# Kernel optimization log

Measured on AMD Instinct MI355X. Metric: run time of the kernel, lower is better.

Reference implementation:

```python
import jax, jax.numpy as jnp
import numpy as np

N_ATOMS, N_UND, N_DIR, N_ANG, N_STRUCT = 8192, 65536, 131072, 262144, 128
FEA, NRAD, NANGB, NCONV = 64, 9, 9, 4

FLOAT_NAMES = ["bond_bases_ag", "bond_bases_bg", "angle_bases", "atom_emb", "Wb", "Wa",
               "Wbw_ag", "Wbw_bg",
               "ac_cw1", "ac_cb1", "ac_cw2", "ac_cb2", "ac_gw1", "ac_gb1", "ac_gw2", "ac_gb2", "ac_out",
               "bc_cw1", "bc_cb1", "bc_cw2", "bc_cb2", "bc_gw1", "bc_gb1", "bc_gw2", "bc_gb2", "bc_out",
               "an_cw", "an_cb", "an_gw", "an_gb",
               "ro_w1", "ro_b1", "ro_w2", "ro_b2", "ro_w3", "ro_b3"]
INT_NAMES = ["atomic_numbers", "atom_graph", "directed2undirected",
             "bond_graph_atoms", "bond_graph_bonds", "atom_owners"]


def _silu(x):
    return x * jax.nn.sigmoid(x)


def _gmlp(x, cw1, cb1, cw2, cb2, gw1, gb1, gw2, gb2):
    # GatedMLP (norm=None): silu(MLP_core(x)) * sigmoid(MLP_gate(x)), each MLP = Lin-silu-Lin
    core = _silu(_silu(x @ cw1 + cb1) @ cw2 + cb2)
    gate = jax.nn.sigmoid(_silu(x @ gw1 + gb1) @ gw2 + gb2)
    return core * gate


def _forward(F, I):
    seg = jax.ops.segment_sum
    atom = F["atom_emb"][I["atomic_numbers"]]            # [N, 64]
    bond = F["bond_bases_ag"] @ F["Wb"]                  # [U, 64]
    angle = F["angle_bases"] @ F["Wa"]                   # [A, 64]
    bw_ag = F["bond_bases_ag"] @ F["Wbw_ag"]             # [U, 64]
    bw_bg = F["bond_bases_bg"] @ F["Wbw_bg"]             # [U, 64]
    ag0, ag1 = I["atom_graph"][:, 0], I["atom_graph"][:, 1]
    d2u = I["directed2undirected"]
    bgi, bgj = I["bond_graph_bonds"][:, 0], I["bond_graph_bonds"][:, 1]
    bga = I["bond_graph_atoms"]

    def atom_conv(i, atom, bond):
        msg = jnp.concatenate([atom[ag0], bond[d2u], atom[ag1]], axis=1)   # [E, 192]
        msg = _gmlp(msg, F["ac_cw1"][i], F["ac_cb1"][i], F["ac_cw2"][i], F["ac_cb2"][i],
                    F["ac_gw1"][i], F["ac_gb1"][i], F["ac_gw2"][i], F["ac_gb2"][i])
        msg = msg * bw_ag[d2u]
        # scatter-add to center atoms, linear mlp_out (no bias), resnet
        return atom + seg(msg, ag0, num_segments=N_ATOMS) @ F["ac_out"][i]

    for i in range(NCONV - 1):
        atom = atom_conv(i, atom, bond)
        # BondConv over bond graph (angles)
        tot = jnp.concatenate([bond[bgi], bond[bgj], angle, atom[bga]], axis=1)  # [A, 256]
        upd = _gmlp(tot, F["bc_cw1"][i], F["bc_cb1"][i], F["bc_cw2"][i], F["bc_cb2"][i],
                    F["bc_gw1"][i], F["bc_gb1"][i], F["bc_gw2"][i], F["bc_gb2"][i])
        upd = upd * bw_bg[bgi]
        bond = bond + seg(upd, bgi, num_segments=N_UND) @ F["bc_out"][i]
        # AngleUpdate (hidden_dim=0 -> single linear in each gated branch), resnet
        tot2 = jnp.concatenate([bond[bgi], bond[bgj], angle, atom[bga]], axis=1)
        angle = angle + _silu(tot2 @ F["an_cw"][i] + F["an_cb"][i]) * \
            jax.nn.sigmoid(tot2 @ F["an_gw"][i] + F["an_gb"][i])
    atom = atom_conv(NCONV - 1, atom, bond)

    # mlp_first readout: per-atom energy MLP then average pooling per structure
    e = _silu(atom @ F["ro_w1"] + F["ro_b1"])
    e = _silu(e @ F["ro_w2"] + F["ro_b2"])
    e = (e @ F["ro_w3"] + F["ro_b3"])[:, 0]              # [N]
    owners = I["atom_owners"]
    esum = seg(e, owners, num_segments=N_STRUCT)
    cnt = seg(jnp.ones_like(e), owners, num_segments=N_STRUCT)
    return esum / jnp.maximum(cnt, 1.0)                  # [N_STRUCT] energy/atom


def setup_inputs() -> dict:
    key = jax.random.key(0)
    ks = iter(jax.random.split(key, 64))

    def nrm(shape, fan_in):
        return jax.random.normal(next(ks), shape, dtype=jnp.float32) / np.float32(np.sqrt(fan_in))

    z = lambda *s: jnp.zeros(s, dtype=jnp.float32)
    inp = {}
    inp["atomic_numbers"] = jax.random.randint(next(ks), (N_ATOMS,), 0, 94, dtype=jnp.int32)
    inp["bond_bases_ag"] = jax.random.uniform(next(ks), (N_UND, NRAD), dtype=jnp.float32)
    inp["bond_bases_bg"] = jax.random.uniform(next(ks), (N_UND, NRAD), dtype=jnp.float32)
    inp["angle_bases"] = jax.random.uniform(next(ks), (N_ANG, NANGB), dtype=jnp.float32)
    inp["atom_graph"] = jax.random.randint(next(ks), (N_DIR, 2), 0, N_ATOMS, dtype=jnp.int32)
    inp["directed2undirected"] = jax.random.randint(next(ks), (N_DIR,), 0, N_UND, dtype=jnp.int32)
    inp["bond_graph_atoms"] = jax.random.randint(next(ks), (N_ANG,), 0, N_ATOMS, dtype=jnp.int32)
    inp["bond_graph_bonds"] = jax.random.randint(next(ks), (N_ANG, 2), 0, N_UND, dtype=jnp.int32)
    inp["atom_owners"] = jnp.sort(jax.random.randint(next(ks), (N_ATOMS,), 0, N_STRUCT, dtype=jnp.int32))
    inp["atom_emb"] = nrm((95, FEA), 1.0)
    inp["Wb"] = nrm((NRAD, FEA), NRAD)
    inp["Wa"] = nrm((NANGB, FEA), NANGB)
    inp["Wbw_ag"] = nrm((NRAD, FEA), NRAD)
    inp["Wbw_bg"] = nrm((NRAD, FEA), NRAD)
    d_a, d_b = 3 * FEA, 4 * FEA
    nb = NCONV - 1
    inp["ac_cw1"] = nrm((NCONV, d_a, FEA), d_a); inp["ac_cb1"] = z(NCONV, FEA)
    inp["ac_cw2"] = nrm((NCONV, FEA, FEA), FEA); inp["ac_cb2"] = z(NCONV, FEA)
    inp["ac_gw1"] = nrm((NCONV, d_a, FEA), d_a); inp["ac_gb1"] = z(NCONV, FEA)
    inp["ac_gw2"] = nrm((NCONV, FEA, FEA), FEA); inp["ac_gb2"] = z(NCONV, FEA)
    inp["ac_out"] = nrm((NCONV, FEA, FEA), FEA)
    inp["bc_cw1"] = nrm((nb, d_b, FEA), d_b); inp["bc_cb1"] = z(nb, FEA)
    inp["bc_cw2"] = nrm((nb, FEA, FEA), FEA); inp["bc_cb2"] = z(nb, FEA)
    inp["bc_gw1"] = nrm((nb, d_b, FEA), d_b); inp["bc_gb1"] = z(nb, FEA)
    inp["bc_gw2"] = nrm((nb, FEA, FEA), FEA); inp["bc_gb2"] = z(nb, FEA)
    inp["bc_out"] = nrm((nb, FEA, FEA), FEA)
    inp["an_cw"] = nrm((nb, d_b, FEA), d_b); inp["an_cb"] = z(nb, FEA)
    inp["an_gw"] = nrm((nb, d_b, FEA), d_b); inp["an_gb"] = z(nb, FEA)
    inp["ro_w1"] = nrm((FEA, FEA), FEA); inp["ro_b1"] = z(FEA)
    inp["ro_w2"] = nrm((FEA, FEA), FEA); inp["ro_b2"] = z(FEA)
    inp["ro_w3"] = nrm((FEA, 1), FEA); inp["ro_b3"] = z(1)
    return inp


def reference(atomic_numbers, bond_bases_ag, bond_bases_bg, angle_bases, atom_graph,
              directed2undirected, bond_graph_atoms, bond_graph_bonds, atom_owners,
              atom_emb, Wb, Wa, Wbw_ag, Wbw_bg,
              ac_cw1, ac_cb1, ac_cw2, ac_cb2, ac_gw1, ac_gb1, ac_gw2, ac_gb2, ac_out,
              bc_cw1, bc_cb1, bc_cw2, bc_cb2, bc_gw1, bc_gb1, bc_gw2, bc_gb2, bc_out,
              an_cw, an_cb, an_gw, an_gb,
              ro_w1, ro_b1, ro_w2, ro_b2, ro_w3, ro_b3):
    loc = locals()
    F = {k: loc[k] for k in FLOAT_NAMES}
    I = {k: loc[k] for k in INT_NAMES}
    return _forward(F, I)
```

## Files before the change

kernel.cpp:

```cpp
#include <hip/hip_runtime.h>
#include <hip/hip_bf16.h>

typedef float f32x4 __attribute__((ext_vector_type(4)));
typedef short s16x8 __attribute__((ext_vector_type(8)));
typedef unsigned int u32x4 __attribute__((ext_vector_type(4)));

#define DEV static __device__ __forceinline__

DEV unsigned short f2bf(float x){
    unsigned u = __builtin_bit_cast(unsigned, x);
    u += 0x7FFFu + ((u >> 16) & 1u);
    return (unsigned short)(u >> 16);
}
DEV float bf2f(unsigned short h){
    unsigned u = ((unsigned)h) << 16;
    return __builtin_bit_cast(float, u);
}
DEV float sigm_(float x){ return __builtin_amdgcn_rcpf(1.0f + __expf(-x)); }
DEV float silu_(float x){ return x * sigm_(x); }

__global__ __launch_bounds__(256) void k_transconv(const float* __restrict__ src,
                                                   unsigned short* __restrict__ dst,
                                                   int K, int total){
    int gid = blockIdx.x * 256 + threadIdx.x;
    if (gid >= total) return;
    int kn  = K * 64;
    int b   = gid / kn;
    int rem = gid - b * kn;
    int k   = rem >> 6, n = rem & 63;
    dst[b * kn + n * K + k] = f2bf(src[gid]);
}

__global__ __launch_bounds__(256) void k_embed(const float* __restrict__ emb,
                                               const int* __restrict__ z,
                                               unsigned short* __restrict__ out){
    int gid = blockIdx.x * 256 + threadIdx.x;
    int n = gid >> 6, f = gid & 63;
    out[gid] = f2bf(emb[z[n] * 64 + f]);
}

__global__ __launch_bounds__(256) void k_smallmm(const float* __restrict__ bases,
                                                 const float* __restrict__ W,
                                                 unsigned short* __restrict__ out){
    int gid = blockIdx.x * 256 + threadIdx.x;
    int r = gid >> 6, f = gid & 63;
    const float* b = bases + r * 9;
    float acc = 0.f;
    #pragma unroll
    for (int k = 0; k < 9; ++k) acc += b[k] * W[k * 64 + f];
    out[gid] = f2bf(acc);
}

__global__ void k_count(const int* __restrict__ dst, int stride, int n, int* __restrict__ cnt){
    int i = blockIdx.x * 256 + threadIdx.x;
    if (i < n) atomicAdd(&cnt[dst[(size_t)i * stride]], 1);
}

__global__ __launch_bounds__(256) void k_bsum(const int* __restrict__ cnt,
                                              int* __restrict__ bsum){
    int i = blockIdx.x * 256 + threadIdx.x;
    int v = cnt[i];
    #pragma unroll
    for (int off = 32; off > 0; off >>= 1) v += __shfl_down(v, off);
    __shared__ int ws[4];
    if ((threadIdx.x & 63) == 0) ws[threadIdx.x >> 6] = v;
    __syncthreads();
    if (threadIdx.x == 0) bsum[blockIdx.x] = ws[0] + ws[1] + ws[2] + ws[3];
}

__global__ __launch_bounds__(256) void k_bscan(const int* __restrict__ bsum,
                                               int* __restrict__ bbase, int nb,
                                               int* __restrict__ total_out){
    __shared__ int sh[256];
    int t = threadIdx.x;
    int v = (t < nb) ? bsum[t] : 0;
    sh[t] = v;
    __syncthreads();
    for (int d = 1; d < 256; d <<= 1){
        int u = (t >= d) ? sh[t - d] : 0;
        __syncthreads();
        sh[t] += u;
        __syncthreads();
    }
    if (t < nb) bbase[t] = sh[t] - v;
    if (t == nb - 1) *total_out = sh[t];
}

__global__ __launch_bounds__(256) void k_offs(const int* __restrict__ cnt,
                                              const int* __restrict__ bbase,
                                              int* __restrict__ offs){
    __shared__ int sh[256];
    int t = threadIdx.x;
    int i = blockIdx.x * 256 + t;
    int v = cnt[i];
    sh[t] = v;
    __syncthreads();
    for (int d = 1; d < 256; d <<= 1){
        int u = (t >= d) ? sh[t - d] : 0;
        __syncthreads();
        sh[t] += u;
        __syncthreads();
    }
    offs[i] = bbase[blockIdx.x] + sh[t] - v;
}

__global__ void k_fill(const int* __restrict__ dst, int stride, int n,
                       const int* __restrict__ offs, int* __restrict__ cur,
                       int* __restrict__ idx){
    int i = blockIdx.x * 256 + threadIdx.x;
    if (i < n){
        int d = dst[(size_t)i * stride];
        int p = offs[d] + atomicAdd(&cur[d], 1);
        idx[p] = i;
    }
}

__global__ __launch_bounds__(256) void k_reduce(const unsigned short* __restrict__ upd,
                                                const int* __restrict__ offs,
                                                const int* __restrict__ idx,
                                                unsigned short* __restrict__ act, int nRows){
    int gid = blockIdx.x * 256 + threadIdx.x;
    int row = gid >> 3;
    if (row >= nRows) return;
    int c8 = (gid & 7) * 8;
    int o = offs[row], e = offs[row + 1];
    float acc[8] = {};
    for (int j = o; j < e; ++j){
        s16x8 v = *(const s16x8*)&upd[(size_t)idx[j] * 64 + c8];
        #pragma unroll
        for (int q = 0; q < 8; ++q) acc[q] += bf2f((unsigned short)v[q]);
    }
    s16x8 a = *(s16x8*)&act[(size_t)row * 64 + c8];
    #pragma unroll
    for (int q = 0; q < 8; ++q) a[q] = (short)f2bf(bf2f((unsigned short)a[q]) + acc[q]);
    *(s16x8*)&act[(size_t)row * 64 + c8] = a;
}

#define MFMA16(a,b,c) __builtin_amdgcn_mfma_f32_16x16x32_bf16(a,b,c,0,0,0)

__global__ __launch_bounds__(256, 4) void k_atom_conv(
    const unsigned short* __restrict__ atomBf, const unsigned short* __restrict__ bondBf,
    const unsigned short* __restrict__ bwagBf,
    const int* __restrict__ agraph, const int* __restrict__ d2u,
    const unsigned short* __restrict__ w1cT, const unsigned short* __restrict__ w1gT,
    const unsigned short* __restrict__ w2cT, const unsigned short* __restrict__ w2gT,
    const unsigned short* __restrict__ woT,
    const float* __restrict__ cb1, const float* __restrict__ cb2,
    const float* __restrict__ gb1, const float* __restrict__ gb2,
    unsigned short* __restrict__ upd)
{
    __shared__ unsigned short lds[14208];
    __shared__ int ldsIdx[64];
    unsigned short* ldsA  = lds;
    unsigned short* ldsHC = lds;
    unsigned short* ldsHG = lds + 4736;
    unsigned short* ldsV  = lds + 9472;
    const int tid = threadIdx.x;
    const int r0  = blockIdx.x * 64;

    {
        const int srow = tid >> 2, q = tid & 3;
        int e = r0 + srow;
        if (q < 3){
            const unsigned short* src;
            if (q == 0)      src = atomBf + (size_t)agraph[2 * e] * 64;
            else if (q == 1){ int u = d2u[e]; ldsIdx[srow] = u; src = bondBf + (size_t)u * 64; }
            else             src = atomBf + (size_t)agraph[2 * e + 1] * 64;
            #pragma unroll
            for (int j = 0; j < 8; ++j)
                *(u32x4*)&ldsA[srow * 200 + q * 64 + j * 8] = *(const u32x4*)(src + j * 8);
        }
    }
    __syncthreads();

    const int lane = tid & 63;
    const int r16  = lane & 15;
    const int grp  = lane >> 4;
    const int col  = (tid >> 6) * 16 + r16;

    unsigned short bwv[16];
    #pragma unroll
    for (int mt = 0; mt < 4; ++mt)
        #pragma unroll
        for (int j = 0; j < 4; ++j)
            bwv[mt * 4 + j] = bwagBf[(size_t)ldsIdx[mt * 16 + grp * 4 + j] * 64 + col];

    f32x4 aC[4] = {}, aG[4] = {};
    #pragma unroll
    for (int kt = 0; kt < 6; ++kt){
        s16x8 bc = *(const s16x8*)&w1cT[col * 192 + kt * 32 + grp * 8];
        s16x8 bg = *(const s16x8*)&w1gT[col * 192 + kt * 32 + grp * 8];
        #pragma unroll
        for (int mt = 0; mt < 4; ++mt){
            s16x8 a = *(const s16x8*)&ldsA[(mt * 16 + r16) * 200 + kt * 32 + grp * 8];
            aC[mt] = MFMA16(a, bc, aC[mt]);
            aG[mt] = MFMA16(a, bg, aG[mt]);
        }
    }
    __syncthreads();

    const float bC1 = cb1[col], bG1 = gb1[col];
    #pragma unroll
    for (int mt = 0; mt < 4; ++mt){
        #pragma unroll
        for (int j = 0; j < 4; ++j){
            int row = mt * 16 + grp * 4 + j;
            ldsHC[row * 74 + col] = f2bf(silu_(aC[mt][j] + bC1));
            ldsHG[row * 74 + col] = f2bf(silu_(aG[mt][j] + bG1));
        }
    }
    __syncthreads();

    f32x4 oC[4] = {}, oG[4] = {};
    #pragma unroll
    for (int kt = 0; kt < 2; ++kt){
        s16x8 bc = *(const s16x8*)&w2cT[col * 64 + kt * 32 + grp * 8];
        s16x8 bg = *(const s16x8*)&w2gT[col * 64 + kt * 32 + grp * 8];
        #pragma unroll
        for (int mt = 0; mt < 4; ++mt){
            s16x8 hc = *(const s16x8*)&ldsHC[(mt * 16 + r16) * 74 + kt * 32 + grp * 8];
            s16x8 hg = *(const s16x8*)&ldsHG[(mt * 16 + r16) * 74 + kt * 32 + grp * 8];
            oC[mt] = MFMA16(hc, bc, oC[mt]);
            oG[mt] = MFMA16(hg, bg, oG[mt]);
        }
    }
    const float bC2 = cb2[col], bG2 = gb2[col];
    #pragma unroll
    for (int mt = 0; mt < 4; ++mt){
        #pragma unroll
        for (int j = 0; j < 4; ++j){
            int row = mt * 16 + grp * 4 + j;
            float v = silu_(oC[mt][j] + bC2) * sigm_(oG[mt][j] + bG2);
            v *= bf2f(bwv[mt * 4 + j]);
            ldsV[row * 74 + col] = f2bf(v);
        }
    }
    __syncthreads();

    f32x4 oD[4] = {};
    #pragma unroll
    for (int kt = 0; kt < 2; ++kt){
        s16x8 bo = *(const s16x8*)&woT[col * 64 + kt * 32 + grp * 8];
        #pragma unroll
        for (int mt = 0; mt < 4; ++mt){
            s16x8 a = *(const s16x8*)&ldsV[(mt * 16 + r16) * 74 + kt * 32 + grp * 8];
            oD[mt] = MFMA16(a, bo, oD[mt]);
        }
    }
    #pragma unroll
    for (int mt = 0; mt < 4; ++mt){
        #pragma unroll
        for (int j = 0; j < 4; ++j){
            int row = mt * 16 + grp * 4 + j;
            upd[(size_t)(r0 + row) * 64 + col] = f2bf(oD[mt][j]);
        }
    }
}

__global__ __launch_bounds__(256, 4) void k_bond_conv(
    const unsigned short* __restrict__ atomBf, const unsigned short* __restrict__ bondBf,
    const unsigned short* __restrict__ angleBf, const unsigned short* __restrict__ bwbgBf,
    const int* __restrict__ bga, const int* __restrict__ bgb,
    const unsigned short* __restrict__ w1cT, const unsigned short* __restrict__ w1gT,
    const unsigned short* __restrict__ w2cT, const unsigned short* __restrict__ w2gT,
    const unsigned short* __restrict__ woT,
    const float* __restrict__ cb1, const float* __restrict__ cb2,
    const float* __restrict__ gb1, const float* __restrict__ gb2,
    unsigned short* __restrict__ upd)
{
    __shared__ unsigned short lds[16896];
    __shared__ int ldsIdx[64];
    unsigned short* ldsA  = lds;
    unsigned short* ldsHC = lds;
    unsigned short* ldsHG = lds + 4736;
    unsigned short* ldsV  = lds + 9472;
    const int tid = threadIdx.x;
    const int r0  = blockIdx.x * 64;

    {
        const int srow = tid >> 2, q = tid & 3;
        int a = r0 + srow;
        const unsigned short* src;
        if (q == 0){ int2 bb = *(const int2*)&bgb[2 * a]; ldsIdx[srow] = bb.x;
                     src = bondBf + (size_t)bb.x * 64; }
        else if (q == 1){ src = bondBf  + (size_t)bgb[2 * a + 1] * 64; }
        else if (q == 2){ src = angleBf + (size_t)a * 64; }
        else            { src = atomBf  + (size_t)bga[a] * 64; }
        #pragma unroll
        for (int j = 0; j < 8; ++j)
            *(u32x4*)&ldsA[srow * 264 + q * 64 + j * 8] = *(const u32x4*)(src + j * 8);
    }
    __syncthreads();

    const int lane = tid & 63;
    const int r16  = lane & 15;
    const int grp  = lane >> 4;
    const int col  = (tid >> 6) * 16 + r16;

    unsigned short bwv[16];
    #pragma unroll
    for (int mt = 0; mt < 4; ++mt)
        #pragma unroll
        for (int j = 0; j < 4; ++j)
            bwv[mt * 4 + j] = bwbgBf[(size_t)ldsIdx[mt * 16 + grp * 4 + j] * 64 + col];

    f32x4 aC[4] = {}, aG[4] = {};
    #pragma unroll
    for (int kt = 0; kt < 8; ++kt){
        s16x8 bc = *(const s16x8*)&w1cT[col * 256 + kt * 32 + grp * 8];
        s16x8 bg = *(const s16x8*)&w1gT[col * 256 + kt * 32 + grp * 8];
        #pragma unroll
        for (int mt = 0; mt < 4; ++mt){
            s16x8 a = *(const s16x8*)&ldsA[(mt * 16 + r16) * 264 + kt * 32 + grp * 8];
            aC[mt] = MFMA16(a, bc, aC[mt]);
            aG[mt] = MFMA16(a, bg, aG[mt]);
        }
    }
    __syncthreads();

    const float bC1 = cb1[col], bG1 = gb1[col];
    #pragma unroll
    for (int mt = 0; mt < 4; ++mt){
        #pragma unroll
        for (int j = 0; j < 4; ++j){
            int row = mt * 16 + grp * 4 + j;
            ldsHC[row * 74 + col] = f2bf(silu_(aC[mt][j] + bC1));
            ldsHG[row * 74 + col] = f2bf(silu_(aG[mt][j] + bG1));
        }
    }
    __syncthreads();

    f32x4 oC[4] = {}, oG[4] = {};
    #pragma unroll
    for (int kt = 0; kt < 2; ++kt){
        s16x8 bc = *(const s16x8*)&w2cT[col * 64 + kt * 32 + grp * 8];
        s16x8 bg = *(const s16x8*)&w2gT[col * 64 + kt * 32 + grp * 8];
        #pragma unroll
        for (int mt = 0; mt < 4; ++mt){
            s16x8 hc = *(const s16x8*)&ldsHC[(mt * 16 + r16) * 74 + kt * 32 + grp * 8];
            s16x8 hg = *(const s16x8*)&ldsHG[(mt * 16 + r16) * 74 + kt * 32 + grp * 8];
            oC[mt] = MFMA16(hc, bc, oC[mt]);
            oG[mt] = MFMA16(hg, bg, oG[mt]);
        }
    }
    const float bC2 = cb2[col], bG2 = gb2[col];
    #pragma unroll
    for (int mt = 0; mt < 4; ++mt){
        #pragma unroll
        for (int j = 0; j < 4; ++j){
            int row = mt * 16 + grp * 4 + j;
            float v = silu_(oC[mt][j] + bC2) * sigm_(oG[mt][j] + bG2);
            v *= bf2f(bwv[mt * 4 + j]);
            ldsV[row * 74 + col] = f2bf(v);
        }
    }
    __syncthreads();

    f32x4 oD[4] = {};
    #pragma unroll
    for (int kt = 0; kt < 2; ++kt){
        s16x8 bo = *(const s16x8*)&woT[col * 64 + kt * 32 + grp * 8];
        #pragma unroll
        for (int mt = 0; mt < 4; ++mt){
            s16x8 a = *(const s16x8*)&ldsV[(mt * 16 + r16) * 74 + kt * 32 + grp * 8];
            oD[mt] = MFMA16(a, bo, oD[mt]);
        }
    }
    #pragma unroll
    for (int mt = 0; mt < 4; ++mt){
        #pragma unroll
        for (int j = 0; j < 4; ++j){
            int row = mt * 16 + grp * 4 + j;
            upd[(size_t)(r0 + row) * 64 + col] = f2bf(oD[mt][j]);
        }
    }
}

__global__ __launch_bounds__(256, 4) void k_angle(
    const unsigned short* __restrict__ atomBf, const unsigned short* __restrict__ bondBf,
    unsigned short* __restrict__ angleBf,
    const int* __restrict__ bga, const int* __restrict__ bgb,
    const unsigned short* __restrict__ wcT, const unsigned short* __restrict__ wgT,
    const float* __restrict__ cb, const float* __restrict__ gb)
{
    __shared__ unsigned short ldsA[64 * 264];
    const int tid = threadIdx.x;
    const int r0  = blockIdx.x * 64;

    {
        const int srow = tid >> 2, q = tid & 3;
        int a = r0 + srow;
        const unsigned short* src;
        if (q == 0)      src = bondBf  + (size_t)bgb[2 * a] * 64;
        else if (q == 1) src = bondBf  + (size_t)bgb[2 * a + 1] * 64;
        else if (q == 2) src = angleBf + (size_t)a * 64;
        else             src = atomBf  + (size_t)bga[a] * 64;
        #pragma unroll
        for (int j = 0; j < 8; ++j)
            *(u32x4*)&ldsA[srow * 264 + q * 64 + j * 8] = *(const u32x4*)(src + j * 8);
    }
    __syncthreads();

    const int lane = tid & 63;
    const int r16  = lane & 15;
    const int grp  = lane >> 4;
    const int col  = (tid >> 6) * 16 + r16;

    f32x4 aC[4] = {}, aG[4] = {};
    #pragma unroll
    for (int kt = 0; kt < 8; ++kt){
        s16x8 bc = *(const s16x8*)&wcT[col * 256 + kt * 32 + grp * 8];
        s16x8 bg = *(const s16x8*)&wgT[col * 256 + kt * 32 + grp * 8];
        #pragma unroll
        for (int mt = 0; mt < 4; ++mt){
            s16x8 a = *(const s16x8*)&ldsA[(mt * 16 + r16) * 264 + kt * 32 + grp * 8];
            aC[mt] = MFMA16(a, bc, aC[mt]);
            aG[mt] = MFMA16(a, bg, aG[mt]);
        }
    }
    const float bC = cb[col], bG = gb[col];
    #pragma unroll
    for (int mt = 0; mt < 4; ++mt){
        #pragma unroll
        for (int j = 0; j < 4; ++j){
            int row = mt * 16 + grp * 4 + j;
            int a = r0 + row;
            float oldv = bf2f(ldsA[row * 264 + 128 + col]);
            float v = silu_(aC[mt][j] + bC) * sigm_(aG[mt][j] + bG);
            angleBf[(size_t)a * 64 + col] = f2bf(oldv + v);
        }
    }
}

__global__ __launch_bounds__(256) void k_readout(
    const unsigned short* __restrict__ atomBf, const int* __restrict__ owners,
    const float* __restrict__ w1, const float* __restrict__ b1,
    const float* __restrict__ w2, const float* __restrict__ b2,
    const float* __restrict__ w3, const float* __restrict__ b3,
    float* __restrict__ esum, float* __restrict__ cnt)
{
    int gid  = blockIdx.x * 256 + threadIdx.x;
    int n    = gid >> 6;
    int lane = threadIdx.x & 63;
    float a = bf2f(atomBf[n * 64 + lane]);
    float acc = b1[lane];
    #pragma unroll
    for (int k = 0; k < 64; ++k) acc += __shfl(a, k) * w1[k * 64 + lane];
    float h = silu_(acc);
    acc = b2[lane];
    #pragma unroll
    for (int k = 0; k < 64; ++k) acc += __shfl(h, k) * w2[k * 64 + lane];
    h = silu_(acc);
    float p = h * w3[lane];
    #pragma unroll
    for (int off = 32; off > 0; off >>= 1) p += __shfl_xor(p, off);
    if (lane == 0){
        atomicAdd(&esum[owners[n]], p + b3[0]);
        atomicAdd(&cnt[owners[n]], 1.0f);
    }
}

__global__ void k_final(const float* __restrict__ esum, const float* __restrict__ cnt,
                        float* __restrict__ out){
    int i = threadIdx.x;
    if (i < 128) out[i] = esum[i] / fmaxf(cnt[i], 1.0f);
}

extern "C" void kernel_launch(void* const* d_in, const int* in_sizes, int n_in,
                              void* d_out, int out_size, void* d_ws, size_t ws_size,
                              hipStream_t stream)
{
    (void)in_sizes; (void)n_in; (void)out_size; (void)ws_size;
    const int N_ATOMS = 8192, N_UND = 65536, N_DIR = 131072, N_ANG = 262144;

    const int*   atomic_numbers = (const int*)  d_in[0];
    const float* bb_ag  = (const float*)d_in[1];
    const float* bb_bg  = (const float*)d_in[2];
    const float* ang_b  = (const float*)d_in[3];
    const int*   agraph = (const int*)  d_in[4];
    const int*   d2u    = (const int*)  d_in[5];
    const int*   bga    = (const int*)  d_in[6];
    const int*   bgb    = (const int*)  d_in[7];
    const int*   owners = (const int*)  d_in[8];
    const float* emb    = (const float*)d_in[9];
    const float* Wb     = (const float*)d_in[10];
    const float* Wa     = (const float*)d_in[11];
    const float* Wbwag  = (const float*)d_in[12];
    const float* Wbwbg  = (const float*)d_in[13];
    const float* ac_cw1 = (const float*)d_in[14];
    const float* ac_cb1 = (const float*)d_in[15];
    const float* ac_cw2 = (const float*)d_in[16];
    const float* ac_cb2 = (const float*)d_in[17];
    const float* ac_gw1 = (const float*)d_in[18];
    const float* ac_gb1 = (const float*)d_in[19];
    const float* ac_gw2 = (const float*)d_in[20];
    const float* ac_gb2 = (const float*)d_in[21];
    const float* ac_out = (const float*)d_in[22];
    const float* bc_cw1 = (const float*)d_in[23];
    const float* bc_cb1 = (const float*)d_in[24];
    const float* bc_cw2 = (const float*)d_in[25];
    const float* bc_cb2 = (const float*)d_in[26];
    const float* bc_gw1 = (const float*)d_in[27];
    const float* bc_gb1 = (const float*)d_in[28];
    const float* bc_gw2 = (const float*)d_in[29];
    const float* bc_gb2 = (const float*)d_in[30];
    const float* bc_out = (const float*)d_in[31];
    const float* an_cw  = (const float*)d_in[32];
    const float* an_cb  = (const float*)d_in[33];
    const float* an_gw  = (const float*)d_in[34];
    const float* an_gb  = (const float*)d_in[35];
    const float* ro_w1  = (const float*)d_in[36];
    const float* ro_b1  = (const float*)d_in[37];
    const float* ro_w2  = (const float*)d_in[38];
    const float* ro_b2  = (const float*)d_in[39];
    const float* ro_w3  = (const float*)d_in[40];
    const float* ro_b3  = (const float*)d_in[41];

    char* ws = (char*)d_ws;
    size_t off = 0;
    auto alloc = [&](size_t bytes) -> void* {
        void* p = ws + off;
        off = (off + bytes + 255) & ~(size_t)255;
        return p;
    };
    unsigned short* atomBf  = (unsigned short*)alloc((size_t)N_ATOMS * 64 * 2);
    unsigned short* bondBf  = (unsigned short*)alloc((size_t)N_UND   * 64 * 2);
    unsigned short* angleBf = (unsigned short*)alloc((size_t)N_ANG   * 64 * 2);
    unsigned short* bwagBf  = (unsigned short*)alloc((size_t)N_UND   * 64 * 2);
    unsigned short* bwbgBf  = (unsigned short*)alloc((size_t)N_UND   * 64 * 2);
    unsigned short* updBuf  = (unsigned short*)alloc((size_t)N_ANG   * 64 * 2);
    float* esum   = (float*)alloc(128 * 4);
    float* cnt    = (float*)alloc(128 * 4);
    int* offsA = (int*)alloc((N_ATOMS + 1) * 4);
    int* curA  = (int*)alloc(N_ATOMS * 4);
    int* idxA  = (int*)alloc((size_t)N_DIR * 4);
    int* offsB = (int*)alloc((N_UND + 1) * 4);
    int* curB  = (int*)alloc(N_UND * 4);
    int* idxB  = (int*)alloc((size_t)N_ANG * 4);
    int* bsum  = (int*)alloc(256 * 4);
    int* bbase = (int*)alloc(256 * 4);
    unsigned short* acw1cT = (unsigned short*)alloc((size_t)4 * 64 * 192 * 2);
    unsigned short* acw1gT = (unsigned short*)alloc((size_t)4 * 64 * 192 * 2);
    unsigned short* acw2cT = (unsigned short*)alloc((size_t)4 * 64 * 64 * 2);
    unsigned short* acw2gT = (unsigned short*)alloc((size_t)4 * 64 * 64 * 2);
    unsigned short* acoT   = (unsigned short*)alloc((size_t)4 * 64 * 64 * 2);
    unsigned short* bcw1cT = (unsigned short*)alloc((size_t)3 * 64 * 256 * 2);
    unsigned short* bcw1gT = (unsigned short*)alloc((size_t)3 * 64 * 256 * 2);
    unsigned short* bcw2cT = (unsigned short*)alloc((size_t)3 * 64 * 64 * 2);
    unsigned short* bcw2gT = (unsigned short*)alloc((size_t)3 * 64 * 64 * 2);
    unsigned short* bcoT   = (unsigned short*)alloc((size_t)3 * 64 * 64 * 2);
    unsigned short* anwcT  = (unsigned short*)alloc((size_t)3 * 64 * 256 * 2);
    unsigned short* anwgT  = (unsigned short*)alloc((size_t)3 * 64 * 256 * 2);

    auto tc = [&](const float* src, unsigned short* dst, int B, int K){
        int total = B * K * 64;
        k_transconv<<<(total + 255) / 256, 256, 0, stream>>>(src, dst, K, total);
    };
    tc(ac_cw1, acw1cT, 4, 192);  tc(ac_gw1, acw1gT, 4, 192);
    tc(ac_cw2, acw2cT, 4, 64);   tc(ac_gw2, acw2gT, 4, 64);
    tc(ac_out, acoT,   4, 64);
    tc(bc_cw1, bcw1cT, 3, 256);  tc(bc_gw1, bcw1gT, 3, 256);
    tc(bc_cw2, bcw2cT, 3, 64);   tc(bc_gw2, bcw2gT, 3, 64);
    tc(bc_out, bcoT,   3, 64);
    tc(an_cw,  anwcT,  3, 256);  tc(an_gw,  anwgT,  3, 256);

    k_embed<<<N_ATOMS * 64 / 256, 256, 0, stream>>>(emb, atomic_numbers, atomBf);
    k_smallmm<<<N_UND * 64 / 256, 256, 0, stream>>>(bb_ag, Wb,    bondBf);
    k_smallmm<<<N_ANG * 64 / 256, 256, 0, stream>>>(ang_b, Wa,    angleBf);
    k_smallmm<<<N_UND * 64 / 256, 256, 0, stream>>>(bb_ag, Wbwag, bwagBf);
    k_smallmm<<<N_UND * 64 / 256, 256, 0, stream>>>(bb_bg, Wbwbg, bwbgBf);

    hipMemsetAsync(curA, 0, N_ATOMS * 4, stream);
    k_count<<<(N_DIR + 255) / 256, 256, 0, stream>>>(agraph, 2, N_DIR, curA);
    k_bsum <<<N_ATOMS / 256, 256, 0, stream>>>(curA, bsum);
    k_bscan<<<1, 256, 0, stream>>>(bsum, bbase, N_ATOMS / 256, offsA + N_ATOMS);
    k_offs <<<N_ATOMS / 256, 256, 0, stream>>>(curA, bbase, offsA);
    hipMemsetAsync(curA, 0, N_ATOMS * 4, stream);
    k_fill<<<(N_DIR + 255) / 256, 256, 0, stream>>>(agraph, 2, N_DIR, offsA, curA, idxA);

    hipMemsetAsync(curB, 0, N_UND * 4, stream);
    k_count<<<(N_ANG + 255) / 256, 256, 0, stream>>>(bgb, 2, N_ANG, curB);
    k_bsum <<<N_UND / 256, 256, 0, stream>>>(curB, bsum);
    k_bscan<<<1, 256, 0, stream>>>(bsum, bbase, N_UND / 256, offsB + N_UND);
    k_offs <<<N_UND / 256, 256, 0, stream>>>(curB, bbase, offsB);
    hipMemsetAsync(curB, 0, N_UND * 4, stream);
    k_fill<<<(N_ANG + 255) / 256, 256, 0, stream>>>(bgb, 2, N_ANG, offsB, curB, idxB);

    for (int i = 0; i < 4; ++i){
        k_atom_conv<<<N_DIR / 64, 256, 0, stream>>>(
            atomBf, bondBf, bwagBf, agraph, d2u,
            acw1cT + (size_t)i * 64 * 192, acw1gT + (size_t)i * 64 * 192,
            acw2cT + (size_t)i * 64 * 64,  acw2gT + (size_t)i * 64 * 64,
            acoT   + (size_t)i * 64 * 64,
            ac_cb1 + i * 64, ac_cb2 + i * 64, ac_gb1 + i * 64, ac_gb2 + i * 64, updBuf);
        k_reduce<<<N_ATOMS * 8 / 256, 256, 0, stream>>>(updBuf, offsA, idxA, atomBf, N_ATOMS);
        if (i == 3) break;
        k_bond_conv<<<N_ANG / 64, 256, 0, stream>>>(
            atomBf, bondBf, angleBf, bwbgBf, bga, bgb,
            bcw1cT + (size_t)i * 64 * 256, bcw1gT + (size_t)i * 64 * 256,
            bcw2cT + (size_t)i * 64 * 64,  bcw2gT + (size_t)i * 64 * 64,
            bcoT   + (size_t)i * 64 * 64,
            bc_cb1 + i * 64, bc_cb2 + i * 64, bc_gb1 + i * 64, bc_gb2 + i * 64, updBuf);
        k_reduce<<<N_UND * 8 / 256, 256, 0, stream>>>(updBuf, offsB, idxB, bondBf, N_UND);
        k_angle<<<N_ANG / 64, 256, 0, stream>>>(
            atomBf, bondBf, angleBf, bga, bgb,
            anwcT + (size_t)i * 64 * 256, anwgT + (size_t)i * 64 * 256,
            an_cb + i * 64, an_gb + i * 64);
    }

    hipMemsetAsync(esum, 0, 128 * 4, stream);
    hipMemsetAsync(cnt,  0, 128 * 4, stream);
    k_readout<<<N_ATOMS * 64 / 256, 256, 0, stream>>>(
        atomBf, owners, ro_w1, ro_b1, ro_w2, ro_b2, ro_w3, ro_b3, esum, cnt);
    k_final<<<1, 128, 0, stream>>>(esum, cnt, (float*)d_out);
}
```

Baseline: 913.2 us.

## Process edges in sorted-destination order and restructure convs to per-wave 16-row tiles

The atom, bond and angle conv kernels now read their rows through the CSR permutation (idxA/idxB), so updates are written contiguously in destination-sorted order. The reduce kernel can then sum a contiguous range without the indirect index load. The kernels are also restructured so each wave owns 16 rows across all 64 output columns, which removes most block-level barriers. In exchange there is an extra indirection on the gather side and more global weight loads per wave.

Measured after the change: 1.481 ms. +62.2%, slower.

```diff
diff --git a/kernel.cpp b/kernel.cpp
--- a/kernel.cpp
+++ b/kernel.cpp
@@ -117,7 +117,6 @@
 
 __global__ __launch_bounds__(256) void k_reduce(const unsigned short* __restrict__ upd,
                                                 const int* __restrict__ offs,
-                                                const int* __restrict__ idx,
                                                 unsigned short* __restrict__ act, int nRows){
     int gid = blockIdx.x * 256 + threadIdx.x;
     int row = gid >> 3;
@@ -126,7 +125,7 @@
     int o = offs[row], e = offs[row + 1];
     float acc[8] = {};
     for (int j = o; j < e; ++j){
-        s16x8 v = *(const s16x8*)&upd[(size_t)idx[j] * 64 + c8];
+        s16x8 v = *(const s16x8*)&upd[(size_t)j * 64 + c8];
         #pragma unroll
         for (int q = 0; q < 8; ++q) acc[q] += bf2f((unsigned short)v[q]);
     }
@@ -142,6 +141,7 @@
     const unsigned short* __restrict__ atomBf, const unsigned short* __restrict__ bondBf,
     const unsigned short* __restrict__ bwagBf,
     const int* __restrict__ agraph, const int* __restrict__ d2u,
+    const int* __restrict__ idxA,
     const unsigned short* __restrict__ w1cT, const unsigned short* __restrict__ w1gT,
     const unsigned short* __restrict__ w2cT, const unsigned short* __restrict__ w2gT,
     const unsigned short* __restrict__ woT,
@@ -149,110 +149,101 @@
     const float* __restrict__ gb1, const float* __restrict__ gb2,
     unsigned short* __restrict__ upd)
 {
-    __shared__ unsigned short lds[14208];
-    __shared__ int ldsIdx[64];
-    unsigned short* ldsA  = lds;
-    unsigned short* ldsHC = lds;
-    unsigned short* ldsHG = lds + 4736;
-    unsigned short* ldsV  = lds + 9472;
-    const int tid = threadIdx.x;
-    const int r0  = blockIdx.x * 64;
-
-    {
-        const int srow = tid >> 2, q = tid & 3;
-        int e = r0 + srow;
-        if (q < 3){
-            const unsigned short* src;
-            if (q == 0)      src = atomBf + (size_t)agraph[2 * e] * 64;
-            else if (q == 1){ int u = d2u[e]; ldsIdx[srow] = u; src = bondBf + (size_t)u * 64; }
-            else             src = atomBf + (size_t)agraph[2 * e + 1] * 64;
-            #pragma unroll
-            for (int j = 0; j < 8; ++j)
-                *(u32x4*)&ldsA[srow * 200 + q * 64 + j * 8] = *(const u32x4*)(src + j * 8);
-        }
-    }
-    __syncthreads();
-
-    const int lane = tid & 63;
-    const int r16  = lane & 15;
-    const int grp  = lane >> 4;
-    const int col  = (tid >> 6) * 16 + r16;
-
-    unsigned short bwv[16];
-    #pragma unroll
-    for (int mt = 0; mt < 4; ++mt)
-        #pragma unroll
-        for (int j = 0; j < 4; ++j)
-            bwv[mt * 4 + j] = bwagBf[(size_t)ldsIdx[mt * 16 + grp * 4 + j] * 64 + col];
-
+    __shared__ unsigned short ldsA[64 * 200];
+    const int tid   = threadIdx.x;
+    const int lane  = tid & 63, wid = tid >> 6;
+    const int r16   = lane & 15, grp = lane >> 4;
+    const int lane8 = lane & 7;
+    const int wrow0 = blockIdx.x * 64 + wid * 16;
+
+    #pragma unroll
+    for (int p = 0; p < 6; ++p){
+        int cc = p * 8 + (lane >> 3);
+        int row16 = cc & 15, q = cc >> 4;
+        int e = idxA[wrow0 + row16];
+        const unsigned short* src;
+        if (q == 0)      src = atomBf + (size_t)agraph[2 * e] * 64;
+        else if (q == 1) src = bondBf + (size_t)d2u[e] * 64;
+        else             src = atomBf + (size_t)agraph[2 * e + 1] * 64;
+        *(u32x4*)&ldsA[(wid * 16 + row16) * 200 + q * 64 + lane8 * 8] =
+            *(const u32x4*)(src + lane8 * 8);
+    }
+    int ubw[4];
+    #pragma unroll
+    for (int j = 0; j < 4; ++j) ubw[j] = d2u[idxA[wrow0 + grp * 4 + j]];
+
+    float c1b[4], g1b[4], c2b[4], g2b[4];
+    #pragma unroll
+    for (int n = 0; n < 4; ++n){
+        c1b[n] = cb1[n * 16 + r16]; g1b[n] = gb1[n * 16 + r16];
+        c2b[n] = cb2[n * 16 + r16]; g2b[n] = gb2[n * 16 + r16];
+    }
+
+    const unsigned short* Arow = ldsA + (wid * 16 + r16) * 200;
     f32x4 aC[4] = {}, aG[4] = {};
     #pragma unroll
     for (int kt = 0; kt < 6; ++kt){
-        s16x8 bc = *(const s16x8*)&w1cT[col * 192 + kt * 32 + grp * 8];
-        s16x8 bg = *(const s16x8*)&w1gT[col * 192 + kt * 32 + grp * 8];
-        #pragma unroll
-        for (int mt = 0; mt < 4; ++mt){
-            s16x8 a = *(const s16x8*)&ldsA[(mt * 16 + r16) * 200 + kt * 32 + grp * 8];
-            aC[mt] = MFMA16(a, bc, aC[mt]);
-            aG[mt] = MFMA16(a, bg, aG[mt]);
-        }
-    }
-    __syncthreads();
-
-    const float bC1 = cb1[col], bG1 = gb1[col];
-    #pragma unroll
-    for (int mt = 0; mt < 4; ++mt){
+        s16x8 a = *(const s16x8*)&Arow[kt * 32 + grp * 8];
+        #pragma unroll
+        for (int n = 0; n < 4; ++n){
+            s16x8 bc = *(const s16x8*)&w1cT[(n * 16 + r16) * 192 + kt * 32 + grp * 8];
+            s16x8 bg = *(const s16x8*)&w1gT[(n * 16 + r16) * 192 + kt * 32 + grp * 8];
+            aC[n] = MFMA16(a, bc, aC[n]);
+            aG[n] = MFMA16(a, bg, aG[n]);
+        }
+    }
+
+    unsigned short* H = ldsA + wid * 16 * 200;
+    #pragma unroll
+    for (int n = 0; n < 4; ++n){
         #pragma unroll
         for (int j = 0; j < 4; ++j){
-            int row = mt * 16 + grp * 4 + j;
-            ldsHC[row * 74 + col] = f2bf(silu_(aC[mt][j] + bC1));
-            ldsHG[row * 74 + col] = f2bf(silu_(aG[mt][j] + bG1));
-        }
-    }
-    __syncthreads();
+            int row16 = grp * 4 + j;
+            H[row16 * 66 + n * 16 + r16]           = f2bf(silu_(aC[n][j] + c1b[n]));
+            H[16 * 66 + row16 * 66 + n * 16 + r16] = f2bf(silu_(aG[n][j] + g1b[n]));
+        }
+    }
 
     f32x4 oC[4] = {}, oG[4] = {};
     #pragma unroll
     for (int kt = 0; kt < 2; ++kt){
-        s16x8 bc = *(const s16x8*)&w2cT[col * 64 + kt * 32 + grp * 8];
-        s16x8 bg = *(const s16x8*)&w2gT[col * 64 + kt * 32 + grp * 8];
-        #pragma unroll
-        for (int mt = 0; mt < 4; ++mt){
-            s16x8 hc = *(const s16x8*)&ldsHC[(mt * 16 + r16) * 74 + kt * 32 + grp * 8];
-            s16x8 hg = *(const s16x8*)&ldsHG[(mt * 16 + r16) * 74 + kt * 32 + grp * 8];
-            oC[mt] = MFMA16(hc, bc, oC[mt]);
-            oG[mt] = MFMA16(hg, bg, oG[mt]);
-        }
-    }
-    const float bC2 = cb2[col], bG2 = gb2[col];
-    #pragma unroll
-    for (int mt = 0; mt < 4; ++mt){
+        s16x8 hc = *(const s16x8*)&H[r16 * 66 + kt * 32 + grp * 8];
+        s16x8 hg = *(const s16x8*)&H[16 * 66 + r16 * 66 + kt * 32 + grp * 8];
+        #pragma unroll
+        for (int n = 0; n < 4; ++n){
+            s16x8 bc = *(const s16x8*)&w2cT[(n * 16 + r16) * 64 + kt * 32 + grp * 8];
+            s16x8 bg = *(const s16x8*)&w2gT[(n * 16 + r16) * 64 + kt * 32 + grp * 8];
+            oC[n] = MFMA16(hc, bc, oC[n]);
+            oG[n] = MFMA16(hg, bg, oG[n]);
+        }
+    }
+    #pragma unroll
+    for (int n = 0; n < 4; ++n){
         #pragma unroll
         for (int j = 0; j < 4; ++j){
-            int row = mt * 16 + grp * 4 + j;
-            float v = silu_(oC[mt][j] + bC2) * sigm_(oG[mt][j] + bG2);
-            v *= bf2f(bwv[mt * 4 + j]);
-            ldsV[row * 74 + col] = f2bf(v);
-        }
-    }
-    __syncthreads();
+            int row16 = grp * 4 + j;
+            float v = silu_(oC[n][j] + c2b[n]) * sigm_(oG[n][j] + g2b[n]);
+            v *= bf2f(bwagBf[(size_t)ubw[j] * 64 + n * 16 + r16]);
+            H[32 * 66 + row16 * 66 + n * 16 + r16] = f2bf(v);
+        }
+    }
 
     f32x4 oD[4] = {};
     #pragma unroll
     for (int kt = 0; kt < 2; ++kt){
-        s16x8 bo = *(const s16x8*)&woT[col * 64 + kt * 32 + grp * 8];
-        #pragma unroll
-        for (int mt = 0; mt < 4; ++mt){
-            s16x8 a = *(const s16x8*)&ldsV[(mt * 16 + r16) * 74 + kt * 32 + grp * 8];
-            oD[mt] = MFMA16(a, bo, oD[mt]);
-        }
-    }
-    #pragma unroll
-    for (int mt = 0; mt < 4; ++mt){
+        s16x8 a = *(const s16x8*)&H[32 * 66 + r16 * 66 + kt * 32 + grp * 8];
+        #pragma unroll
+        for (int n = 0; n < 4; ++n){
+            s16x8 bo = *(const s16x8*)&woT[(n * 16 + r16) * 64 + kt * 32 + grp * 8];
+            oD[n] = MFMA16(a, bo, oD[n]);
+        }
+    }
+    #pragma unroll
+    for (int n = 0; n < 4; ++n){
         #pragma unroll
         for (int j = 0; j < 4; ++j){
-            int row = mt * 16 + grp * 4 + j;
-            upd[(size_t)(r0 + row) * 64 + col] = f2bf(oD[mt][j]);
+            int r = wrow0 + grp * 4 + j;
+            upd[(size_t)r * 64 + n * 16 + r16] = f2bf(oD[n][j]);
         }
     }
 }
@@ -261,6 +252,7 @@
     const unsigned short* __restrict__ atomBf, const unsigned short* __restrict__ bondBf,
     const unsigned short* __restrict__ angleBf, const unsigned short* __restrict__ bwbgBf,
     const int* __restrict__ bga, const int* __restrict__ bgb,
+    const int* __restrict__ idxB,
     const unsigned short* __restrict__ w1cT, const unsigned short* __restrict__ w1gT,
     const unsigned short* __restrict__ w2cT, const unsigned short* __restrict__ w2gT,
     const unsigned short* __restrict__ woT,
@@ -268,166 +260,163 @@
     const float* __restrict__ gb1, const float* __restrict__ gb2,
     unsigned short* __restrict__ upd)
 {
-    __shared__ unsigned short lds[16896];
-    __shared__ int ldsIdx[64];
-    unsigned short* ldsA  = lds;
-    unsigned short* ldsHC = lds;
-    unsigned short* ldsHG = lds + 4736;
-    unsigned short* ldsV  = lds + 9472;
-    const int tid = threadIdx.x;
-    const int r0  = blockIdx.x * 64;
-
-    {
-        const int srow = tid >> 2, q = tid & 3;
-        int a = r0 + srow;
-        const unsigned short* src;
-        if (q == 0){ int2 bb = *(const int2*)&bgb[2 * a]; ldsIdx[srow] = bb.x;
-                     src = bondBf + (size_t)bb.x * 64; }
-        else if (q == 1){ src = bondBf  + (size_t)bgb[2 * a + 1] * 64; }
-        else if (q == 2){ src = angleBf + (size_t)a * 64; }
-        else            { src = atomBf  + (size_t)bga[a] * 64; }
-        #pragma unroll
-        for (int j = 0; j < 8; ++j)
-            *(u32x4*)&ldsA[srow * 264 + q * 64 + j * 8] = *(const u32x4*)(src + j * 8);
-    }
-    __syncthreads();
-
-    const int lane = tid & 63;
-    const int r16  = lane & 15;
-    const int grp  = lane >> 4;
-    const int col  = (tid >> 6) * 16 + r16;
-
-    unsigned short bwv[16];
-    #pragma unroll
-    for (int mt = 0; mt < 4; ++mt)
-        #pragma unroll
-        for (int j = 0; j < 4; ++j)
-            bwv[mt * 4 + j] = bwbgBf[(size_t)ldsIdx[mt * 16 + grp * 4 + j] * 64 + col];
-
-    f32x4 aC[4] = {}, aG[4] = {};
-    #pragma unroll
-    for (int kt = 0; kt < 8; ++kt){
-        s16x8 bc = *(const s16x8*)&w1cT[col * 256 + kt * 32 + grp * 8];
-        s16x8 bg = *(const s16x8*)&w1gT[col * 256 + kt * 32 + grp * 8];
-        #pragma unroll
-        for (int mt = 0; mt < 4; ++mt){
-            s16x8 a = *(const s16x8*)&ldsA[(mt * 16 + r16) * 264 + kt * 32 + grp * 8];
-            aC[mt] = MFMA16(a, bc, aC[mt]);
-            aG[mt] = MFMA16(a, bg, aG[mt]);
-        }
-    }
-    __syncthreads();
-
-    const float bC1 = cb1[col], bG1 = gb1[col];
-    #pragma unroll
-    for (int mt = 0; mt < 4; ++mt){
-        #pragma unroll
-        for (int j = 0; j < 4; ++j){
-            int row = mt * 16 + grp * 4 + j;
-            ldsHC[row * 74 + col] = f2bf(silu_(aC[mt][j] + bC1));
-            ldsHG[row * 74 + col] = f2bf(silu_(aG[mt][j] + bG1));
-        }
-    }
-    __syncthreads();
-
-    f32x4 oC[4] = {}, oG[4] = {};
-    #pragma unroll
-    for (int kt = 0; kt < 2; ++kt){
-        s16x8 bc = *(const s16x8*)&w2cT[col * 64 + kt * 32 + grp * 8];
-        s16x8 bg = *(const s16x8*)&w2gT[col * 64 + kt * 32 + grp * 8];
-        #pragma unroll
-        for (int mt = 0; mt < 4; ++mt){
-            s16x8 hc = *(const s16x8*)&ldsHC[(mt * 16 + r16) * 74 + kt * 32 + grp * 8];
-            s16x8 hg = *(const s16x8*)&ldsHG[(mt * 16 + r16) * 74 + kt * 32 + grp * 8];
-            oC[mt] = MFMA16(hc, bc, oC[mt]);
-            oG[mt] = MFMA16(hg, bg, oG[mt]);
-        }
-    }
-    const float bC2 = cb2[col], bG2 = gb2[col];
-    #pragma unroll
-    for (int mt = 0; mt < 4; ++mt){
-        #pragma unroll
-        for (int j = 0; j < 4; ++j){
-            int row = mt * 16 + grp * 4 + j;
-            float v = silu_(oC[mt][j] + bC2) * sigm_(oG[mt][j] + bG2);
-            v *= bf2f(bwv[mt * 4 + j]);
-            ldsV[row * 74 + col] = f2bf(v);
-        }
-    }
-    __syncthreads();
-
-    f32x4 oD[4] = {};
-    #pragma unroll
-    for (int kt = 0; kt < 2; ++kt){
-        s16x8 bo = *(const s16x8*)&woT[col * 64 + kt * 32 + grp * 8];
-        #pragma unroll
-        for (int mt = 0; mt < 4; ++mt){
-            s16x8 a = *(const s16x8*)&ldsV[(mt * 16 + r16) * 74 + kt * 32 + grp * 8];
-            oD[mt] = MFMA16(a, bo, oD[mt]);
-        }
-    }
-    #pragma unroll
-    for (int mt = 0; mt < 4; ++mt){
-        #pragma unroll
-        for (int j = 0; j < 4; ++j){
-            int row = mt * 16 + grp * 4 + j;
-            upd[(size_t)(r0 + row) * 64 + col] = f2bf(oD[mt][j]);
-        }
-    }
-}
-
-__global__ __launch_bounds__(256, 4) void k_angle(
-    const unsigned short* __restrict__ atomBf, const unsigned short* __restrict__ bondBf,
-    unsigned short* __restrict__ angleBf,
-    const int* __restrict__ bga, const int* __restrict__ bgb,
-    const unsigned short* __restrict__ wcT, const unsigned short* __restrict__ wgT,
-    const float* __restrict__ cb, const float* __restrict__ gb)
-{
     __shared__ unsigned short ldsA[64 * 264];
-    const int tid = threadIdx.x;
-    const int r0  = blockIdx.x * 64;
-
-    {
-        const int srow = tid >> 2, q = tid & 3;
-        int a = r0 + srow;
+    const int tid   = threadIdx.x;
+    const int lane  = tid & 63, wid = tid >> 6;
+    const int r16   = lane & 15, grp = lane >> 4;
+    const int lane8 = lane & 7;
+    const int wrow0 = blockIdx.x * 64 + wid * 16;
+
+    #pragma unroll
+    for (int p = 0; p < 8; ++p){
+        int cc = p * 8 + (lane >> 3);
+        int row16 = cc & 15, q = cc >> 4;
+        int a = idxB[wrow0 + row16];
         const unsigned short* src;
         if (q == 0)      src = bondBf  + (size_t)bgb[2 * a] * 64;
         else if (q == 1) src = bondBf  + (size_t)bgb[2 * a + 1] * 64;
         else if (q == 2) src = angleBf + (size_t)a * 64;
         else             src = atomBf  + (size_t)bga[a] * 64;
-        #pragma unroll
-        for (int j = 0; j < 8; ++j)
-            *(u32x4*)&ldsA[srow * 264 + q * 64 + j * 8] = *(const u32x4*)(src + j * 8);
-    }
-    __syncthreads();
-
-    const int lane = tid & 63;
-    const int r16  = lane & 15;
-    const int grp  = lane >> 4;
-    const int col  = (tid >> 6) * 16 + r16;
-
+        *(u32x4*)&ldsA[(wid * 16 + row16) * 264 + q * 64 + lane8 * 8] =
+            *(const u32x4*)(src + lane8 * 8);
+    }
+    int ubw[4];
+    #pragma unroll
+    for (int j = 0; j < 4; ++j) ubw[j] = bgb[2 * idxB[wrow0 + grp * 4 + j]];
+
+    float c1b[4], g1b[4], c2b[4], g2b[4];
+    #pragma unroll
+    for (int n = 0; n < 4; ++n){
+        c1b[n] = cb1[n * 16 + r16]; g1b[n] = gb1[n * 16 + r16];
+        c2b[n] = cb2[n * 16 + r16]; g2b[n] = gb2[n * 16 + r16];
+    }
+
+    const unsigned short* Arow = ldsA + (wid * 16 + r16) * 264;
     f32x4 aC[4] = {}, aG[4] = {};
     #pragma unroll
     for (int kt = 0; kt < 8; ++kt){
-        s16x8 bc = *(const s16x8*)&wcT[col * 256 + kt * 32 + grp * 8];
-        s16x8 bg = *(const s16x8*)&wgT[col * 256 + kt * 32 + grp * 8];
-        #pragma unroll
-        for (int mt = 0; mt < 4; ++mt){
-            s16x8 a = *(const s16x8*)&ldsA[(mt * 16 + r16) * 264 + kt * 32 + grp * 8];
-            aC[mt] = MFMA16(a, bc, aC[mt]);
-            aG[mt] = MFMA16(a, bg, aG[mt]);
-        }
-    }
-    const float bC = cb[col], bG = gb[col];
-    #pragma unroll
-    for (int mt = 0; mt < 4; ++mt){
+        s16x8 a = *(const s16x8*)&Arow[kt * 32 + grp * 8];
+        #pragma unroll
+        for (int n = 0; n < 4; ++n){
+            s16x8 bc = *(const s16x8*)&w1cT[(n * 16 + r16) * 256 + kt * 32 + grp * 8];
+            s16x8 bg = *(const s16x8*)&w1gT[(n * 16 + r16) * 256 + kt * 32 + grp * 8];
+            aC[n] = MFMA16(a, bc, aC[n]);
+            aG[n] = MFMA16(a, bg, aG[n]);
+        }
+    }
+
+    unsigned short* H = ldsA + wid * 16 * 264;
+    #pragma unroll
+    for (int n = 0; n < 4; ++n){
         #pragma unroll
         for (int j = 0; j < 4; ++j){
-            int row = mt * 16 + grp * 4 + j;
-            int a = r0 + row;
-            float oldv = bf2f(ldsA[row * 264 + 128 + col]);
-            float v = silu_(aC[mt][j] + bC) * sigm_(aG[mt][j] + bG);
-            angleBf[(size_t)a * 64 + col] = f2bf(oldv + v);
+            int row16 = grp * 4 + j;
+            H[row16 * 74 + n * 16 + r16]           = f2bf(silu_(aC[n][j] + c1b[n]));
+            H[16 * 74 + row16 * 74 + n * 16 + r16] = f2bf(silu_(aG[n][j] + g1b[n]));
+        }
+    }
+
+    f32x4 oC[4] = {}, oG[4] = {};
+    #pragma unroll
+    for (int kt = 0; kt < 2; ++kt){
+        s16x8 hc = *(const s16x8*)&H[r16 * 74 + kt * 32 + grp * 8];
+        s16x8 hg = *(const s16x8*)&H[16 * 74 + r16 * 74 + kt * 32 + grp * 8];
+        #pragma unroll
+        for (int n = 0; n < 4; ++n){
+            s16x8 bc = *(const s16x8*)&w2cT[(n * 16 + r16) * 64 + kt * 32 + grp * 8];
+            s16x8 bg = *(const s16x8*)&w2gT[(n * 16 + r16) * 64 + kt * 32 + grp * 8];
+            oC[n] = MFMA16(hc, bc, oC[n]);
+            oG[n] = MFMA16(hg, bg, oG[n]);
+        }
+    }
+    #pragma unroll
+    for (int n = 0; n < 4; ++n){
+        #pragma unroll
+        for (int j = 0; j < 4; ++j){
+            int row16 = grp * 4 + j;
+            float v = silu_(oC[n][j] + c2b[n]) * sigm_(oG[n][j] + g2b[n]);
+            v *= bf2f(bwbgBf[(size_t)ubw[j] * 64 + n * 16 + r16]);
+            H[32 * 74 + row16 * 74 + n * 16 + r16] = f2bf(v);
+        }
+    }
+
+    f32x4 oD[4] = {};
+    #pragma unroll
+    for (int kt = 0; kt < 2; ++kt){
+        s16x8 a = *(const s16x8*)&H[32 * 74 + r16 * 74 + kt * 32 + grp * 8];
+        #pragma unroll
+        for (int n = 0; n < 4; ++n){
+            s16x8 bo = *(const s16x8*)&woT[(n * 16 + r16) * 64 + kt * 32 + grp * 8];
+            oD[n] = MFMA16(a, bo, oD[n]);
+        }
+    }
+    #pragma unroll
+    for (int n = 0; n < 4; ++n){
+        #pragma unroll
+        for (int j = 0; j < 4; ++j){
+            int r = wrow0 + grp * 4 + j;
+            upd[(size_t)r * 64 + n * 16 + r16] = f2bf(oD[n][j]);
+        }
+    }
+}
+
+__global__ __launch_bounds__(256, 4) void k_angle(
+    const unsigned short* __restrict__ atomBf, const unsigned short* __restrict__ bondBf,
+    unsigned short* __restrict__ angleBf,
+    const int* __restrict__ bga, const int* __restrict__ bgb,
+    const int* __restrict__ idxB,
+    const unsigned short* __restrict__ wcT, const unsigned short* __restrict__ wgT,
+    const float* __restrict__ cb, const float* __restrict__ gb)
+{
+    __shared__ unsigned short ldsA[64 * 264];
+    const int tid   = threadIdx.x;
+    const int lane  = tid & 63, wid = tid >> 6;
+    const int r16   = lane & 15, grp = lane >> 4;
+    const int lane8 = lane & 7;
+    const int wrow0 = blockIdx.x * 64 + wid * 16;
+
+    #pragma unroll
+    for (int p = 0; p < 8; ++p){
+        int cc = p * 8 + (lane >> 3);
+        int row16 = cc & 15, q = cc >> 4;
+        int a = idxB[wrow0 + row16];
+        const unsigned short* src;
+        if (q == 0)      src = bondBf  + (size_t)bgb[2 * a] * 64;
+        else if (q == 1) src = bondBf  + (size_t)bgb[2 * a + 1] * 64;
+        else if (q == 2) src = angleBf + (size_t)a * 64;
+        else             src = atomBf  + (size_t)bga[a] * 64;
+        *(u32x4*)&ldsA[(wid * 16 + row16) * 264 + q * 64 + lane8 * 8] =
+            *(const u32x4*)(src + lane8 * 8);
+    }
+    int aid[4];
+    #pragma unroll
+    for (int j = 0; j < 4; ++j) aid[j] = idxB[wrow0 + grp * 4 + j];
+
+    float cbv[4], gbv[4];
+    #pragma unroll
+    for (int n = 0; n < 4; ++n){ cbv[n] = cb[n * 16 + r16]; gbv[n] = gb[n * 16 + r16]; }
+
+    const unsigned short* Arow = ldsA + (wid * 16 + r16) * 264;
+    f32x4 aC[4] = {}, aG[4] = {};
+    #pragma unroll
+    for (int kt = 0; kt < 8; ++kt){
+        s16x8 a = *(const s16x8*)&Arow[kt * 32 + grp * 8];
+        #pragma unroll
+        for (int n = 0; n < 4; ++n){
+            s16x8 bc = *(const s16x8*)&wcT[(n * 16 + r16) * 256 + kt * 32 + grp * 8];
+            s16x8 bg = *(const s16x8*)&wgT[(n * 16 + r16) * 256 + kt * 32 + grp * 8];
+            aC[n] = MFMA16(a, bc, aC[n]);
+            aG[n] = MFMA16(a, bg, aG[n]);
+        }
+    }
+    #pragma unroll
+    for (int n = 0; n < 4; ++n){
+        #pragma unroll
+        for (int j = 0; j < 4; ++j){
+            int row16 = grp * 4 + j;
+            float oldv = bf2f(ldsA[(wid * 16 + row16) * 264 + 128 + n * 16 + r16]);
+            float v = silu_(aC[n][j] + cbv[n]) * sigm_(aG[n][j] + gbv[n]);
+            angleBf[(size_t)aid[j] * 64 + n * 16 + r16] = f2bf(oldv + v);
         }
     }
 }
@@ -588,22 +577,22 @@
 
     for (int i = 0; i < 4; ++i){
         k_atom_conv<<<N_DIR / 64, 256, 0, stream>>>(
-            atomBf, bondBf, bwagBf, agraph, d2u,
+            atomBf, bondBf, bwagBf, agraph, d2u, idxA,
             acw1cT + (size_t)i * 64 * 192, acw1gT + (size_t)i * 64 * 192,
             acw2cT + (size_t)i * 64 * 64,  acw2gT + (size_t)i * 64 * 64,
             acoT   + (size_t)i * 64 * 64,
             ac_cb1 + i * 64, ac_cb2 + i * 64, ac_gb1 + i * 64, ac_gb2 + i * 64, updBuf);
-        k_reduce<<<N_ATOMS * 8 / 256, 256, 0, stream>>>(updBuf, offsA, idxA, atomBf, N_ATOMS);
+        k_reduce<<<N_ATOMS * 8 / 256, 256, 0, stream>>>(updBuf, offsA, atomBf, N_ATOMS);
         if (i == 3) break;
         k_bond_conv<<<N_ANG / 64, 256, 0, stream>>>(
-            atomBf, bondBf, angleBf, bwbgBf, bga, bgb,
+            atomBf, bondBf, angleBf, bwbgBf, bga, bgb, idxB,
             bcw1cT + (size_t)i * 64 * 256, bcw1gT + (size_t)i * 64 * 256,
             bcw2cT + (size_t)i * 64 * 64,  bcw2gT + (size_t)i * 64 * 64,
             bcoT   + (size_t)i * 64 * 64,
             bc_cb1 + i * 64, bc_cb2 + i * 64, bc_gb1 + i * 64, bc_gb2 + i * 64, updBuf);
-        k_reduce<<<N_UND * 8 / 256, 256, 0, stream>>>(updBuf, offsB, idxB, bondBf, N_UND);
+        k_reduce<<<N_UND * 8 / 256, 256, 0, stream>>>(updBuf, offsB, bondBf, N_UND);
         k_angle<<<N_ANG / 64, 256, 0, stream>>>(
-            atomBf, bondBf, angleBf, bga, bgb,
+            atomBf, bondBf, angleBf, bga, bgb, idxB,
             anwcT + (size_t)i * 64 * 256, anwgT + (size_t)i * 64 * 256,
             an_cb + i * 64, an_gb + i * 64);
     }
```
